# Optimization experiments

Hardware: AMD Instinct MI355X
Metric: run time of the kernel (lower is better)

The kernel has to match this reference:

```python
import jax, jax.numpy as jnp
import numpy as np
from jax import lax

N_NODES, N_EDGES, N_GRAPHS = 102400, 409600, 2048
HID, BN_EPS = 128, 1e-5


def setup_inputs():
    kit = iter(jax.random.split(jax.random.key(0), 64))

    def nrm(shape, s=0.02):
        return jax.random.normal(next(kit), shape, jnp.float32) * s

    inp = {}
    inp["x_ligand"] = jax.random.normal(next(kit), (N_NODES, 78), jnp.float32)
    inp["protein_seq"] = jax.random.normal(next(kit), (N_GRAPHS, 1, 1000), jnp.float32)
    inp["a2h"] = jax.random.normal(next(kit), (N_GRAPHS, 10, 100, 3), jnp.float32)
    inp["edge_index"] = jax.random.randint(next(kit), (2, N_EDGES), 0, N_NODES)
    inp["batch_ligand"] = jnp.sort(jax.random.randint(next(kit), (N_NODES,), 0, N_GRAPHS))
    dins = [78, HID, HID]
    for i in range(3):
        inp[f"gin{i}_W1"] = nrm((dins[i], HID)); inp[f"gin{i}_b1"] = jnp.zeros((HID,), jnp.float32)
        inp[f"gin{i}_W2"] = nrm((HID, HID)); inp[f"gin{i}_b2"] = jnp.zeros((HID,), jnp.float32)
        inp[f"bn{i}_g"] = jnp.ones((HID,), jnp.float32); inp[f"bn{i}_b"] = jnp.zeros((HID,), jnp.float32)
    inp["lig_W"] = nrm((HID, HID)); inp["lig_b"] = jnp.zeros((HID,), jnp.float32)
    inp["conv_k"] = nrm((32, 1, 8)); inp["conv_b"] = jnp.zeros((32,), jnp.float32)
    inp["prot_W"] = nrm((32, HID)); inp["prot_b"] = jnp.zeros((HID,), jnp.float32)
    inp["a2h1_W"] = nrm((3000, HID)); inp["a2h1_b"] = jnp.zeros((HID,), jnp.float32)
    inp["a2h2_W"] = nrm((HID, HID)); inp["a2h2_b"] = jnp.zeros((HID,), jnp.float32)
    inp["c1_W"] = nrm((3 * HID, 2 * HID)); inp["c1_b"] = jnp.zeros((2 * HID,), jnp.float32)
    inp["c2_W"] = nrm((2 * HID, HID)); inp["c2_b"] = jnp.zeros((HID,), jnp.float32)
    inp["out_W"] = nrm((HID, 1)); inp["out_b"] = jnp.zeros((1,), jnp.float32)
    return inp


def _gin_layer(x, src, dst, W1, b1, W2, b2, g, b):
    # scatter-add neighbor aggregation (PyG GINConv, eps=0)
    agg = jax.ops.segment_sum(x[src], dst, num_segments=N_NODES)
    h = x + agg
    h = jax.nn.relu(h @ W1 + b1) @ W2 + b2  # GIN MLP
    mu = h.mean(0)
    var = h.var(0)
    h = (h - mu) * lax.rsqrt(var + BN_EPS) * g + b  # BatchNorm1d (batch stats)
    return jax.nn.relu(h)


def _forward(x_ligand, protein_seq, a2h, edge_index, batch_ligand, gin_params,
             lig_W, lig_b, conv_k, conv_b, prot_W, prot_b,
             a2h1_W, a2h1_b, a2h2_W, a2h2_b, c1_W, c1_b, c2_W, c2_b, out_W, out_b):
    src, dst = edge_index[0], edge_index[1]
    x = x_ligand
    for (W1, b1, W2, b2, g, b) in gin_params:
        x = _gin_layer(x, src, dst, W1, b1, W2, b2, g, b)
    xg = jax.ops.segment_sum(x, batch_ligand, num_segments=N_GRAPHS)  # global_add_pool
    xg = jax.nn.relu(xg @ lig_W + lig_b)
    # protein CNN branch: Conv1d(1->32, k=8) + ReLU + global max pool
    xp = lax.conv_general_dilated(protein_seq, conv_k, (1,), 'VALID',
                                  dimension_numbers=('NCH', 'OIH', 'NCH')) + conv_b[None, :, None]
    xp = jax.nn.relu(xp).max(axis=-1)
    xp = jax.nn.relu(xp @ prot_W + prot_b)
    # a2h MLP branch on flattened trajectory
    xa = a2h.reshape(a2h.shape[0], -1)
    xa = jax.nn.relu(xa @ a2h1_W + a2h1_b)
    xa = jax.nn.relu(xa @ a2h2_W + a2h2_b)
    xc = jnp.concatenate([xg, xp, xa], axis=1)
    xc = jax.nn.relu(xc @ c1_W + c1_b)
    xc = jax.nn.relu(xc @ c2_W + c2_b)
    return xc @ out_W + out_b


def reference(x_ligand, protein_seq, a2h, edge_index, batch_ligand,
              gin0_W1, gin0_b1, gin0_W2, gin0_b2, bn0_g, bn0_b,
              gin1_W1, gin1_b1, gin1_W2, gin1_b2, bn1_g, bn1_b,
              gin2_W1, gin2_b1, gin2_W2, gin2_b2, bn2_g, bn2_b,
              lig_W, lig_b, conv_k, conv_b, prot_W, prot_b,
              a2h1_W, a2h1_b, a2h2_W, a2h2_b, c1_W, c1_b, c2_W, c2_b, out_W, out_b):
    gin_params = [
        (gin0_W1, gin0_b1, gin0_W2, gin0_b2, bn0_g, bn0_b),
        (gin1_W1, gin1_b1, gin1_W2, gin1_b2, bn1_g, bn1_b),
        (gin2_W1, gin2_b1, gin2_W2, gin2_b2, bn2_g, bn2_b),
    ]
    return _forward(x_ligand, protein_seq, a2h, edge_index, batch_ligand, gin_params,
                    lig_W, lig_b, conv_k, conv_b, prot_W, prot_b,
                    a2h1_W, a2h1_b, a2h2_W, a2h2_b, c1_W, c1_b, c2_W, c2_b, out_W, out_b)
```

## Files before the change

kernel.cpp:

```cpp
#include <hip/hip_runtime.h>
#include <math.h>

constexpr int NNODES  = 102400;
constexpr int NEDGES  = 409600;
constexpr int NGRAPHS = 2048;
constexpr int HIDDEN  = 128;

typedef __attribute__((ext_vector_type(8))) short s16x8;
typedef __attribute__((ext_vector_type(4))) float f32x4;

__device__ __forceinline__ float relu_f(float v) { return fmaxf(v, 0.0f); }

__device__ __forceinline__ void split3(float x, short& s0, short& s1, short& s2) {
  unsigned u0 = __float_as_uint(x);
  s0 = (short)(u0 >> 16);
  float r1 = x - __uint_as_float(u0 & 0xFFFF0000u);
  unsigned u1 = __float_as_uint(r1);
  s1 = (short)(u1 >> 16);
  float r2 = r1 - __uint_as_float(u1 & 0xFFFF0000u);
  s2 = (short)(__float_as_uint(r2) >> 16);
}

__global__ void prep_kernel(const int* __restrict__ ei, const int* __restrict__ batch,
                            int* __restrict__ counts, int* __restrict__ gcounts,
                            const float* __restrict__ W10, const float* __restrict__ W20,
                            const float* __restrict__ W11, const float* __restrict__ W21,
                            const float* __restrict__ W12, const float* __restrict__ W22,
                            short* __restrict__ ws) {
  int b = blockIdx.x;
  if (b < NEDGES / 256) {
    atomicAdd(&counts[ei[NEDGES + b * 256 + threadIdx.x]], 1);
    return;
  }
  if (b < NEDGES / 256 + NNODES / 256) {
    atomicAdd(&gcounts[batch[(b - NEDGES / 256) * 256 + threadIdx.x]], 1);
    return;
  }
  int bw = b - (NEDGES / 256 + NNODES / 256);
  int n = threadIdx.x;
  if (n >= 128) return;
  const float* src; long base; int k, realK, KP;
  if (bw < 96) {
    src = W10; base = 0; k = bw; realK = 78; KP = 96;
  } else {
    int q = bw - 96;
    int mat = q >> 7;
    k = q & 127; realK = 128; KP = 128;
    const float* srcs[5] = {W20, W11, W21, W12, W22};
    const long bases[5] = {36864, 86016, 135168, 184320, 233472};
    src = srcs[mat]; base = bases[mat];
  }
  float x = (k < realK) ? src[k * 128 + n] : 0.0f;
  short s0, s1, s2;
  split3(x, s0, s1, s2);
  long e = base + ((long)(k >> 5) * 128 + n) * 32 + (k & 31);
  long ps = (long)KP * 128;
  ws[e] = s0; ws[e + ps] = s1; ws[e + 2 * ps] = s2;
}

__device__ __forceinline__ void scan_block_body(const int* in, int n, int* out_excl,
                                                int* bsums, int lb) {
  __shared__ int s[256];
  int t = threadIdx.x;
  int i = lb * 256 + t;
  int v = (i < n) ? in[i] : 0;
  s[t] = v;
  __syncthreads();
  for (int off = 1; off < 256; off <<= 1) {
    int x = (t >= off) ? s[t - off] : 0;
    __syncthreads();
    s[t] += x;
    __syncthreads();
  }
  if (i < n) out_excl[i] = s[t] - v;
  if (t == 255) bsums[lb] = s[255];
}

__global__ void scan_block2_kernel(const int* __restrict__ counts, int* __restrict__ row_ptr,
                                   int* __restrict__ bsumsA, const int* __restrict__ gcounts,
                                   int* __restrict__ gptr, int* __restrict__ bsumsB) {
  int b = blockIdx.x;
  if (b < NNODES / 256) scan_block_body(counts, NNODES, row_ptr, bsumsA, b);
  else scan_block_body(gcounts, NGRAPHS, gptr, bsumsB, b - NNODES / 256);
}

__global__ void scan_top2_kernel(int* __restrict__ bsumsA, int* __restrict__ bsumsB) {
  __shared__ int s[1024];
  int* bs = (blockIdx.x == 0) ? bsumsA : bsumsB;
  int nb  = (blockIdx.x == 0) ? (NNODES / 256) : (NGRAPHS / 256);
  int t = threadIdx.x;
  int v = (t < nb) ? bs[t] : 0;
  s[t] = v;
  __syncthreads();
  for (int off = 1; off < 1024; off <<= 1) {
    int x = (t >= off) ? s[t - off] : 0;
    __syncthreads();
    s[t] += x;
    __syncthreads();
  }
  if (t < nb) bs[t] = s[t] - v;
  if (t == 1023) bs[nb] = s[1023];
}

__global__ void scan_add2_kernel(int* __restrict__ row_ptr, const int* __restrict__ bsumsA,
                                 int* __restrict__ nxt, int* __restrict__ gptr,
                                 const int* __restrict__ bsumsB) {
  int b = blockIdx.x, t = threadIdx.x;
  if (b < NNODES / 256) {
    int i = b * 256 + t;
    int v = row_ptr[i] + bsumsA[b];
    row_ptr[i] = v;
    nxt[i] = v;
    if (i == 0) row_ptr[NNODES] = bsumsA[NNODES / 256];
  } else {
    int lb = b - NNODES / 256;
    int i = lb * 256 + t;
    gptr[i] += bsumsB[lb];
    if (i == 0) gptr[NGRAPHS] = bsumsB[NGRAPHS / 256];
  }
}

__global__ void scatter_kernel(const int* __restrict__ ei, int* __restrict__ nxt,
                               int* __restrict__ csr_src) {
  int e = blockIdx.x * blockDim.x + threadIdx.x;
  if (e < NEDGES) {
    int s = ei[e];
    int d = ei[NEDGES + e];
    int pos = atomicAdd(&nxt[d], 1);
    csr_src[pos] = s;
  }
}

constexpr int STRK = 132;
template<int DIN, int KP1, bool XF>
__device__ __forceinline__ void gin_block(
    int bid, const float* __restrict__ X,
    const int* __restrict__ row_ptr, const int* __restrict__ csr_src,
    const short* __restrict__ w1s, const float* __restrict__ b1,
    const short* __restrict__ w2s, const float* __restrict__ b2,
    const float* __restrict__ psum, const float* __restrict__ psq,
    const float* __restrict__ bg, const float* __restrict__ bb2,
    float* __restrict__ O, float* __restrict__ bn_sum, float* __restrict__ bn_sq,
    float* buf) {
  const int t = threadIdx.x;
  const int wv = t >> 6, lane = t & 63;
  const int base = bid * 32;

  const int fp = 2 * lane;
  if (fp < KP1) {
    if (fp < DIN) {
      float sc0 = 1.f, sh0 = 0.f, sc1 = 1.f, sh1 = 0.f;
      if (XF) {
        float mu0 = psum[fp] * (1.0f / NNODES);
        float va0 = fmaxf(psq[fp] * (1.0f / NNODES) - mu0 * mu0, 0.0f);
        sc0 = bg[fp] / sqrtf(va0 + 1e-5f);
        sh0 = bb2[fp] - mu0 * sc0;
        float mu1 = psum[fp + 1] * (1.0f / NNODES);
        float va1 = fmaxf(psq[fp + 1] * (1.0f / NNODES) - mu1 * mu1, 0.0f);
        sc1 = bg[fp + 1] / sqrtf(va1 + 1e-5f);
        sh1 = bb2[fp + 1] - mu1 * sc1;
      }
      for (int g = 0; g < 2; ++g) {
        const int rbase = wv * 8 + g * 4;
        float a0[4], a1[4];
        int ecur[4], eend[4], idx[4];
#pragma unroll
        for (int r = 0; r < 4; ++r) {
          const int node = base + rbase + r;
          ecur[r] = row_ptr[node];
          eend[r] = row_ptr[node + 1];
          const float2 s = *(const float2*)&X[(long)node * DIN + fp];
          a0[r] = XF ? relu_f(fmaf(s.x, sc0, sh0)) : s.x;
          a1[r] = XF ? relu_f(fmaf(s.y, sc1, sh1)) : s.y;
          idx[r] = (ecur[r] < eend[r]) ? csr_src[ecur[r]] : -1;
        }
        bool any = (idx[0] >= 0) || (idx[1] >= 0) || (idx[2] >= 0) || (idx[3] >= 0);
        while (any) {
          float2 uu[4];
#pragma unroll
          for (int r = 0; r < 4; ++r)
            if (idx[r] >= 0) uu[r] = *(const float2*)&X[(long)idx[r] * DIN + fp];
          any = false;
#pragma unroll
          for (int r = 0; r < 4; ++r) {
            if (idx[r] >= 0) {
              a0[r] += XF ? relu_f(fmaf(uu[r].x, sc0, sh0)) : uu[r].x;
              a1[r] += XF ? relu_f(fmaf(uu[r].y, sc1, sh1)) : uu[r].y;
              ++ecur[r];
              idx[r] = (ecur[r] < eend[r]) ? csr_src[ecur[r]] : -1;
            }
            any = any || (idx[r] >= 0);
          }
        }
#pragma unroll
        for (int r = 0; r < 4; ++r)
          *(float2*)&buf[(rbase + r) * STRK + fp] = make_float2(a0[r], a1[r]);
      }
    } else {
      for (int r = 0; r < 8; ++r)
        *(float2*)&buf[(wv * 8 + r) * STRK + fp] = make_float2(0.f, 0.f);
    }
  }
  __syncthreads();

  const int rb = wv & 1, nbase = (wv >> 1) * 64;
  const int l15 = lane & 15, quad = lane >> 4;
  const int aoff = (rb * 16 + l15) * STRK;
  constexpr int PS1 = KP1 * 128;
  constexpr int PS2 = 128 * 128;

  f32x4 acc1[4] = {};
  for (int ks = 0; ks < KP1 / 32; ++ks) {
    const int k0 = ks * 32;
    const float4 xa = *(const float4*)&buf[aoff + k0 + quad * 8];
    const float4 xb = *(const float4*)&buf[aoff + k0 + quad * 8 + 4];
    s16x8 A0, A1, A2;
    {
      const float xv[8] = {xa.x, xa.y, xa.z, xa.w, xb.x, xb.y, xb.z, xb.w};
#pragma unroll
      for (int j = 0; j < 8; ++j) {
        short s0, s1, s2;
        split3(xv[j], s0, s1, s2);
        A0[j] = s0; A1[j] = s1; A2[j] = s2;
      }
    }
    s16x8 B0[4], B1[4], B2[4];
#pragma unroll
    for (int ct = 0; ct < 4; ++ct) {
      const int n = nbase + ct * 16 + l15;
      const short* wp = w1s + ((long)(ks * 128 + n) << 5) + (quad << 3);
      B0[ct] = *(const s16x8*)(wp);
      B1[ct] = *(const s16x8*)(wp + PS1);
      B2[ct] = *(const s16x8*)(wp + 2 * PS1);
    }
#pragma unroll
    for (int ct = 0; ct < 4; ++ct) acc1[ct] = __builtin_amdgcn_mfma_f32_16x16x32_bf16(A0, B2[ct], acc1[ct], 0, 0, 0);
#pragma unroll
    for (int ct = 0; ct < 4; ++ct) acc1[ct] = __builtin_amdgcn_mfma_f32_16x16x32_bf16(A1, B1[ct], acc1[ct], 0, 0, 0);
#pragma unroll
    for (int ct = 0; ct < 4; ++ct) acc1[ct] = __builtin_amdgcn_mfma_f32_16x16x32_bf16(A2, B0[ct], acc1[ct], 0, 0, 0);
#pragma unroll
    for (int ct = 0; ct < 4; ++ct) acc1[ct] = __builtin_amdgcn_mfma_f32_16x16x32_bf16(A0, B1[ct], acc1[ct], 0, 0, 0);
#pragma unroll
    for (int ct = 0; ct < 4; ++ct) acc1[ct] = __builtin_amdgcn_mfma_f32_16x16x32_bf16(A1, B0[ct], acc1[ct], 0, 0, 0);
#pragma unroll
    for (int ct = 0; ct < 4; ++ct) acc1[ct] = __builtin_amdgcn_mfma_f32_16x16x32_bf16(A0, B0[ct], acc1[ct], 0, 0, 0);
  }
  __syncthreads();

#pragma unroll
  for (int ct = 0; ct < 4; ++ct) {
    const int n = nbase + ct * 16 + l15;
    const float bb = b1[n];
#pragma unroll
    for (int reg = 0; reg < 4; ++reg) {
      const int m = rb * 16 + quad * 4 + reg;
      buf[m * STRK + n] = relu_f(acc1[ct][reg] + bb);
    }
  }
  __syncthreads();

  f32x4 acc2[4] = {};
  for (int ks = 0; ks < 4; ++ks) {
    const int k0 = ks * 32;
    const float4 xa = *(const float4*)&buf[aoff + k0 + quad * 8];
    const float4 xb = *(const float4*)&buf[aoff + k0 + quad * 8 + 4];
    s16x8 A0, A1, A2;
    {
      const float xv[8] = {xa.x, xa.y, xa.z, xa.w, xb.x, xb.y, xb.z, xb.w};
#pragma unroll
      for (int j = 0; j < 8; ++j) {
        short s0, s1, s2;
        split3(xv[j], s0, s1, s2);
        A0[j] = s0; A1[j] = s1; A2[j] = s2;
      }
    }
    s16x8 B0[4], B1[4], B2[4];
#pragma unroll
    for (int ct = 0; ct < 4; ++ct) {
      const int n = nbase + ct * 16 + l15;
      const short* wp = w2s + ((long)(ks * 128 + n) << 5) + (quad << 3);
      B0[ct] = *(const s16x8*)(wp);
      B1[ct] = *(const s16x8*)(wp + PS2);
      B2[ct] = *(const s16x8*)(wp + 2 * PS2);
    }
#pragma unroll
    for (int ct = 0; ct < 4; ++ct) acc2[ct] = __builtin_amdgcn_mfma_f32_16x16x32_bf16(A0, B2[ct], acc2[ct], 0, 0, 0);
#pragma unroll
    for (int ct = 0; ct < 4; ++ct) acc2[ct] = __builtin_amdgcn_mfma_f32_16x16x32_bf16(A1, B1[ct], acc2[ct], 0, 0, 0);
#pragma unroll
    for (int ct = 0; ct < 4; ++ct) acc2[ct] = __builtin_amdgcn_mfma_f32_16x16x32_bf16(A2, B0[ct], acc2[ct], 0, 0, 0);
#pragma unroll
    for (int ct = 0; ct < 4; ++ct) acc2[ct] = __builtin_amdgcn_mfma_f32_16x16x32_bf16(A0, B1[ct], acc2[ct], 0, 0, 0);
#pragma unroll
    for (int ct = 0; ct < 4; ++ct) acc2[ct] = __builtin_amdgcn_mfma_f32_16x16x32_bf16(A1, B0[ct], acc2[ct], 0, 0, 0);
#pragma unroll
    for (int ct = 0; ct < 4; ++ct) acc2[ct] = __builtin_amdgcn_mfma_f32_16x16x32_bf16(A0, B0[ct], acc2[ct], 0, 0, 0);
  }

  float cs[4], cq[4];
#pragma unroll
  for (int ct = 0; ct < 4; ++ct) {
    const int n = nbase + ct * 16 + l15;
    const float bb = b2[n];
    float s = 0.f, q = 0.f;
#pragma unroll
    for (int reg = 0; reg < 4; ++reg) {
      const int m = rb * 16 + quad * 4 + reg;
      const float o = acc2[ct][reg] + bb;
      O[(long)(base + m) * HIDDEN + n] = o;
      s += o;
      q = fmaf(o, o, q);
    }
    cs[ct] = s; cq[ct] = q;
  }
  __syncthreads();
  const int g = rb * 4 + quad;
#pragma unroll
  for (int ct = 0; ct < 4; ++ct) {
    const int n = nbase + ct * 16 + l15;
    buf[n * 8 + g] = cs[ct];
    buf[1024 + n * 8 + g] = cq[ct];
  }
  __syncthreads();
  if (t < HIDDEN) {
    float s = 0.f, q = 0.f;
    for (int gg = 0; gg < 8; ++gg) { s += buf[t * 8 + gg]; q += buf[1024 + t * 8 + gg]; }
    atomicAdd(&bn_sum[t], s);
    atomicAdd(&bn_sq[t], q);
  }
}

constexpr int A2H_K = 3000, A2H_SPLIT = 200, A2H_NSPLIT = 15;
__device__ __forceinline__ void a2h_block(int rb, int sp, const float* __restrict__ A,
    const float* __restrict__ W, const float* __restrict__ bias, float* __restrict__ XA,
    float* xT) {
  constexpr int STR = 18;
  const int t = threadIdx.x;
  const int row0 = rb * 16;
  const int k0 = sp * A2H_SPLIT;
  for (int i = t; i < 16 * 50; i += 256) {
    const int r = i / 50, kq = i - r * 50;
    const float4 v = *(const float4*)&A[(long)(row0 + r) * A2H_K + k0 + kq * 4];
    xT[(kq * 4 + 0) * STR + r] = v.x;
    xT[(kq * 4 + 1) * STR + r] = v.y;
    xT[(kq * 4 + 2) * STR + r] = v.z;
    xT[(kq * 4 + 3) * STR + r] = v.w;
  }
  __syncthreads();
  const int rg = t >> 5, cg = t & 31;
  const int r0 = rg * 2, j0 = cg * 4;
  float acc[2][4];
  for (int r = 0; r < 2; ++r)
    for (int c = 0; c < 4; ++c) acc[r][c] = 0.f;
  const float* Wp = W + (long)k0 * HIDDEN + j0;
  for (int k = 0; k < A2H_SPLIT; ++k) {
    const float4 w = *(const float4*)&Wp[(long)k * HIDDEN];
    const float2 x = *(const float2*)&xT[k * STR + r0];
    const float wa[4] = {w.x, w.y, w.z, w.w};
    for (int c = 0; c < 4; ++c) {
      acc[0][c] = fmaf(x.x, wa[c], acc[0][c]);
      acc[1][c] = fmaf(x.y, wa[c], acc[1][c]);
    }
  }
  if (sp == 0)
    for (int c = 0; c < 4; ++c) { acc[0][c] += bias[j0 + c]; acc[1][c] += bias[j0 + c]; }
  for (int r = 0; r < 2; ++r)
    for (int c = 0; c < 4; ++c)
      atomicAdd(&XA[(long)(row0 + r0 + r) * HIDDEN + j0 + c], acc[r][c]);
}

__device__ __forceinline__ void conv_block(int g, const float* __restrict__ PS,
    const float* __restrict__ CK, const float* __restrict__ CB, float* __restrict__ XP,
    float* seq) {
  const int t = threadIdx.x;
  for (int i = t; i < 1000; i += 256) seq[i] = PS[g * 1000 + i];
  __syncthreads();
  const int pl = t & 31, cgp = t >> 5;
  float kr[4][8];
  for (int cc = 0; cc < 4; ++cc)
    for (int k = 0; k < 8; ++k) kr[cc][k] = CK[(cgp * 4 + cc) * 8 + k];
  float m[4] = {-1e30f, -1e30f, -1e30f, -1e30f};
  for (int i = 0; i < 32; ++i) {
    int p = pl + 32 * i;
    if (p < 993) {
      float sv[8];
      for (int k = 0; k < 8; ++k) sv[k] = seq[p + k];
      for (int cc = 0; cc < 4; ++cc) {
        float s = 0.f;
        for (int k = 0; k < 8; ++k) s = fmaf(sv[k], kr[cc][k], s);
        m[cc] = fmaxf(m[cc], s);
      }
    }
  }
  for (int off = 16; off >= 1; off >>= 1)
    for (int cc = 0; cc < 4; ++cc) m[cc] = fmaxf(m[cc], __shfl_xor(m[cc], off));
  if (pl == 0)
    for (int cc = 0; cc < 4; ++cc)
      XP[g * 32 + cgp * 4 + cc] = relu_f(m[cc] + CB[cgp * 4 + cc]);
}

__global__ __launch_bounds__(256, 4) void fat0_kernel(
    const float* __restrict__ x_lig, const int* __restrict__ row_ptr,
    const int* __restrict__ csr_src,
    const short* __restrict__ ws, const float* __restrict__ b1,
    const float* __restrict__ b2,
    float* __restrict__ O0, float* __restrict__ bn_sum, float* __restrict__ bn_sq,
    const float* __restrict__ a2h, const float* __restrict__ a1W,
    const float* __restrict__ a1b, float* __restrict__ XA,
    const float* __restrict__ pseq, const float* __restrict__ convk,
    const float* __restrict__ convb, float* __restrict__ XP32) {
  __shared__ __align__(16) float buf[32 * STRK];
  const int b = blockIdx.x;
  if (b < NNODES / 32) {
    gin_block<78, 96, false>(b, x_lig, row_ptr, csr_src, ws, b1, ws + 36864, b2,
                             nullptr, nullptr, nullptr, nullptr, O0, bn_sum, bn_sq, buf);
  } else if (b < NNODES / 32 + (NGRAPHS / 16) * A2H_NSPLIT) {
    const int q = b - NNODES / 32;
    a2h_block(q & 127, q >> 7, a2h, a1W, a1b, XA, buf);
  } else {
    conv_block(b - (NNODES / 32 + (NGRAPHS / 16) * A2H_NSPLIT), pseq, convk, convb, XP32, buf);
  }
}

__global__ __launch_bounds__(256, 4) void gin_kernel(
    const float* __restrict__ X, const int* __restrict__ row_ptr,
    const int* __restrict__ csr_src,
    const short* __restrict__ w1s, const float* __restrict__ b1,
    const short* __restrict__ w2s, const float* __restrict__ b2,
    const float* __restrict__ psum, const float* __restrict__ psq,
    const float* __restrict__ bg, const float* __restrict__ bb2,
    float* __restrict__ O, float* __restrict__ bn_sum, float* __restrict__ bn_sq) {
  __shared__ __align__(16) float buf[32 * STRK];
  gin_block<128, 128, true>(blockIdx.x, X, row_ptr, csr_src, w1s, b1, w2s, b2,
                            psum, psq, bg, bb2, O, bn_sum, bn_sq, buf);
}

__global__ __launch_bounds__(256) void pool_kernel(const float* __restrict__ O,
    const int* __restrict__ gp, const float* __restrict__ psum, const float* __restrict__ psq,
    const float* __restrict__ bg, const float* __restrict__ bb2, float* __restrict__ P) {
  int t = threadIdx.x;
  int g = blockIdx.x * 4 + (t >> 6);
  int lane = t & 63;
  int f0 = lane, f1 = lane + 64;
  float mu0 = psum[f0] * (1.0f / NNODES);
  float va0 = fmaxf(psq[f0] * (1.0f / NNODES) - mu0 * mu0, 0.0f);
  float sc0 = bg[f0] / sqrtf(va0 + 1e-5f);
  float sh0 = bb2[f0] - mu0 * sc0;
  float mu1 = psum[f1] * (1.0f / NNODES);
  float va1 = fmaxf(psq[f1] * (1.0f / NNODES) - mu1 * mu1, 0.0f);
  float sc1 = bg[f1] / sqrtf(va1 + 1e-5f);
  float sh1 = bb2[f1] - mu1 * sc1;
  int n0 = gp[g], n1 = gp[g + 1];
  float a0 = 0.f, a1 = 0.f;
  for (int n = n0; n < n1; ++n) {
    a0 += relu_f(fmaf(O[(long)n * HIDDEN + f0], sc0, sh0));
    a1 += relu_f(fmaf(O[(long)n * HIDDEN + f1], sc1, sh1));
  }
  P[g * HIDDEN + f0] = a0;
  P[g * HIDDEN + f1] = a1;
}

__device__ __forceinline__ void gemm16_body(const float* __restrict__ A, int lda, int K,
    const float* __restrict__ W, int ldw, const float* __restrict__ bias,
    float* __restrict__ C, int ldc, int coff, int yc, bool reluA, float* AT) {
  constexpr int RT = 16, CH = 64, STR = RT + 4;
  const int t = threadIdx.x;
  const int rg = t >> 6, cg = t & 63;
  const int r0 = rg * 4;
  const int row0 = blockIdx.x * RT;
  const int col = yc * 64 + cg;
  float a0 = 0.f, a1 = 0.f, a2 = 0.f, a3 = 0.f;
  for (int k0 = 0; k0 < K; k0 += CH) {
    const int kc = min(CH, K - k0);
    __syncthreads();
    for (int i = t; i < RT * CH; i += 256) {
      int kk = i & (CH - 1), r = i >> 6;
      if (kk < kc) {
        float v = A[(long)(row0 + r) * lda + k0 + kk];
        AT[kk * STR + r] = reluA ? relu_f(v) : v;
      }
    }
    __syncthreads();
    for (int kk = 0; kk < kc; ++kk) {
      const float4 x = *(const float4*)&AT[kk * STR + r0];
      const float w = W[(long)(k0 + kk) * ldw + col];
      a0 = fmaf(x.x, w, a0);
      a1 = fmaf(x.y, w, a1);
      a2 = fmaf(x.z, w, a2);
      a3 = fmaf(x.w, w, a3);
    }
  }
  const float bv = bias[col];
  C[(long)(row0 + r0 + 0) * ldc + coff + col] = relu_f(a0 + bv);
  C[(long)(row0 + r0 + 1) * ldc + coff + col] = relu_f(a1 + bv);
  C[(long)(row0 + r0 + 2) * ldc + coff + col] = relu_f(a2 + bv);
  C[(long)(row0 + r0 + 3) * ldc + coff + col] = relu_f(a3 + bv);
}

__global__ __launch_bounds__(256) void branches_kernel(
    const float* __restrict__ P, const float* __restrict__ XP32, const float* __restrict__ XA,
    const float* __restrict__ ligW, const float* __restrict__ ligb,
    const float* __restrict__ protW, const float* __restrict__ protb,
    const float* __restrict__ a2W, const float* __restrict__ a2b, float* __restrict__ XC) {
  __shared__ __align__(16) float AT[64 * 20];
  const int cfg = blockIdx.y >> 1, yc = blockIdx.y & 1;
  if (cfg == 0)      gemm16_body(P,    128, 128, ligW,  128, ligb,  XC, 384, 0,   yc, false, AT);
  else if (cfg == 1) gemm16_body(XP32, 32,  32,  protW, 128, protb, XC, 384, 128, yc, false, AT);
  else               gemm16_body(XA,   128, 128, a2W,   128, a2b,   XC, 384, 256, yc, true,  AT);
}

__global__ __launch_bounds__(256) void gemm2_kernel(const float* __restrict__ A, int lda, int K,
    const float* __restrict__ W, int ldw, const float* __restrict__ bias,
    float* __restrict__ C, int ldc) {
  __shared__ __align__(16) float AT[64 * 20];
  gemm16_body(A, lda, K, W, ldw, bias, C, ldc, 0, blockIdx.y, false, AT);
}

__global__ __launch_bounds__(256) void final_dot_kernel(const float* __restrict__ X,
    const float* __restrict__ Wo, const float* __restrict__ bo, float* __restrict__ out) {
  int t = threadIdx.x;
  int g = blockIdx.x * 4 + (t >> 6);
  int lane = t & 63;
  float2 x = *(const float2*)&X[g * HIDDEN + lane * 2];
  float2 w = *(const float2*)&Wo[lane * 2];
  float p = x.x * w.x + x.y * w.y;
  for (int off = 32; off >= 1; off >>= 1) p += __shfl_down(p, off);
  if (lane == 0) out[g] = p + bo[0];
}

extern "C" void kernel_launch(void* const* d_in, const int* in_sizes, int n_in,
                              void* d_out, int out_size, void* d_ws, size_t ws_size,
                              hipStream_t stream) {
  const float* x_lig = (const float*)d_in[0];
  const float* pseq  = (const float*)d_in[1];
  const float* a2h   = (const float*)d_in[2];
  const int*   ei    = (const int*)d_in[3];
  const int*   batch = (const int*)d_in[4];
  const float* ginW1[3] = {(const float*)d_in[5],  (const float*)d_in[11], (const float*)d_in[17]};
  const float* ginb1[3] = {(const float*)d_in[6],  (const float*)d_in[12], (const float*)d_in[18]};
  const float* ginW2[3] = {(const float*)d_in[7],  (const float*)d_in[13], (const float*)d_in[19]};
  const float* ginb2[3] = {(const float*)d_in[8],  (const float*)d_in[14], (const float*)d_in[20]};
  const float* bng[3]   = {(const float*)d_in[9],  (const float*)d_in[15], (const float*)d_in[21]};
  const float* bnb[3]   = {(const float*)d_in[10], (const float*)d_in[16], (const float*)d_in[22]};
  const float* ligW  = (const float*)d_in[23]; const float* ligb  = (const float*)d_in[24];
  const float* convk = (const float*)d_in[25]; const float* convb = (const float*)d_in[26];
  const float* protW = (const float*)d_in[27]; const float* protb = (const float*)d_in[28];
  const float* a1W   = (const float*)d_in[29]; const float* a1b   = (const float*)d_in[30];
  const float* a2W   = (const float*)d_in[31]; const float* a2b   = (const float*)d_in[32];
  const float* c1W   = (const float*)d_in[33]; const float* c1b   = (const float*)d_in[34];
  const float* c2W   = (const float*)d_in[35]; const float* c2b   = (const float*)d_in[36];
  const float* oW    = (const float*)d_in[37]; const float* ob    = (const float*)d_in[38];

  char* base = (char*)d_ws;
  size_t off = 0;
  auto alloc = [&](size_t bytes) -> char* {
    char* p = base + off;
    off = (off + bytes + 511) & ~size_t(511);
    return p;
  };
  int*   counts  = (int*)alloc(NNODES * 4);
  int*   gcounts = (int*)alloc(NGRAPHS * 4);
  float* bn_sum  = (float*)alloc(3 * 128 * 4);
  float* bn_sq   = (float*)alloc(3 * 128 * 4);
  float* XA      = (float*)alloc(NGRAPHS * 128 * 4);
  const size_t zero_bytes = off;
  short* wsplit   = (short*)alloc(282624 * 2);
  int*   row_ptr  = (int*)alloc((NNODES + 1) * 4);
  int*   nxt      = (int*)alloc(NNODES * 4);
  int*   gptr     = (int*)alloc((NGRAPHS + 1) * 4);
  int*   bsumsA   = (int*)alloc(401 * 4);
  int*   bsumsB   = (int*)alloc(9 * 4);
  int*   csr_src  = (int*)alloc(NEDGES * 4);
  float* P        = (float*)alloc(NGRAPHS * 128 * 4);
  float* XP32     = (float*)alloc(NGRAPHS * 32 * 4);
  float* XC       = (float*)alloc(NGRAPHS * 384 * 4);
  float* XC2      = (float*)alloc(NGRAPHS * 256 * 4);
  float* XC3      = (float*)alloc(NGRAPHS * 128 * 4);
  float* O0       = (float*)alloc((size_t)NNODES * 128 * 4);
  float* O1       = (float*)alloc((size_t)NNODES * 128 * 4);
  (void)ws_size; (void)in_sizes; (void)n_in; (void)out_size;

  hipMemsetAsync(d_ws, 0, zero_bytes, stream);

  prep_kernel<<<NEDGES / 256 + NNODES / 256 + 736, 256, 0, stream>>>(
      ei, batch, counts, gcounts, ginW1[0], ginW2[0], ginW1[1], ginW2[1],
      ginW1[2], ginW2[2], wsplit);
  scan_block2_kernel<<<NNODES / 256 + NGRAPHS / 256, 256, 0, stream>>>(
      counts, row_ptr, bsumsA, gcounts, gptr, bsumsB);
  scan_top2_kernel<<<2, 1024, 0, stream>>>(bsumsA, bsumsB);
  scan_add2_kernel<<<NNODES / 256 + NGRAPHS / 256, 256, 0, stream>>>(
      row_ptr, bsumsA, nxt, gptr, bsumsB);
  scatter_kernel<<<(NEDGES + 255) / 256, 256, 0, stream>>>(ei, nxt, csr_src);

  fat0_kernel<<<NNODES / 32 + (NGRAPHS / 16) * A2H_NSPLIT + NGRAPHS, 256, 0, stream>>>(
      x_lig, row_ptr, csr_src, wsplit, ginb1[0], ginb2[0],
      O0, bn_sum, bn_sq, a2h, a1W, a1b, XA, pseq, convk, convb, XP32);

  gin_kernel<<<NNODES / 32, 256, 0, stream>>>(O0, row_ptr, csr_src,
      wsplit + 86016, ginb1[1], wsplit + 135168, ginb2[1],
      bn_sum, bn_sq, bng[0], bnb[0], O1, bn_sum + 128, bn_sq + 128);
  gin_kernel<<<NNODES / 32, 256, 0, stream>>>(O1, row_ptr, csr_src,
      wsplit + 184320, ginb1[2], wsplit + 233472, ginb2[2],
      bn_sum + 128, bn_sq + 128, bng[1], bnb[1], O0, bn_sum + 256, bn_sq + 256);

  pool_kernel<<<NGRAPHS / 4, 256, 0, stream>>>(O0, gptr, bn_sum + 256, bn_sq + 256,
                                               bng[2], bnb[2], P);
  branches_kernel<<<dim3(NGRAPHS / 16, 6), 256, 0, stream>>>(
      P, XP32, XA, ligW, ligb, protW, protb, a2W, a2b, XC);
  gemm2_kernel<<<dim3(NGRAPHS / 16, 4), 256, 0, stream>>>(XC, 384, 384, c1W, 256, c1b, XC2, 256);
  gemm2_kernel<<<dim3(NGRAPHS / 16, 2), 256, 0, stream>>>(XC2, 256, 256, c2W, 128, c2b, XC3, 128);
  final_dot_kernel<<<NGRAPHS / 4, 256, 0, stream>>>(XC3, oW, ob, (float*)d_out);
}
```

Before: 848.3 us.

## Fuse pooling and MLP head into one kernel; widen GIN gather to float4

The five tail kernels (pool, three branch linears, two dense layers, final dot) become a single head kernel that does 4 graphs per block and keeps all intermediates in shared memory. This removes launches and global round-trips for P/XC/XC2/XC3. Layers 1-2 of the GIN gather now use float4 loads, with two nodes per wave, instead of float2 loads. The trade-off is that the head kernel rereads every weight matrix for each group of 4 graphs, with only 512 blocks doing scalar FMA loops.

```diff
diff --git a/kernel.cpp b/kernel.cpp
--- a/kernel.cpp
+++ b/kernel.cpp
@@ -132,7 +132,7 @@
 }
 
 constexpr int STRK = 132;
-template<int DIN, int KP1, bool XF>
+template<int DIN, int KP1, bool XF, bool G4>
 __device__ __forceinline__ void gin_block(
     int bid, const float* __restrict__ X,
     const int* __restrict__ row_ptr, const int* __restrict__ csr_src,
@@ -146,59 +146,106 @@
   const int wv = t >> 6, lane = t & 63;
   const int base = bid * 32;
 
-  const int fp = 2 * lane;
-  if (fp < KP1) {
-    if (fp < DIN) {
-      float sc0 = 1.f, sh0 = 0.f, sc1 = 1.f, sh1 = 0.f;
+  if (G4) {
+    const int q = lane & 31, half = lane >> 5;
+    const int f = 4 * q;
+    float sc[4] = {1.f, 1.f, 1.f, 1.f}, sh[4] = {0.f, 0.f, 0.f, 0.f};
+    if (XF) {
+#pragma unroll
+      for (int c = 0; c < 4; ++c) {
+        float mu = psum[f + c] * (1.0f / NNODES);
+        float va = fmaxf(psq[f + c] * (1.0f / NNODES) - mu * mu, 0.0f);
+        sc[c] = bg[f + c] / sqrtf(va + 1e-5f);
+        sh[c] = bb2[f + c] - mu * sc[c];
+      }
+    }
+    float4 acc[4];
+    int ecur[4], eend[4], idx[4];
+#pragma unroll
+    for (int p = 0; p < 4; ++p) {
+      const int node = base + wv * 8 + 2 * p + half;
+      ecur[p] = row_ptr[node];
+      eend[p] = row_ptr[node + 1];
+      float4 s = *(const float4*)&X[(long)node * 128 + f];
       if (XF) {
-        float mu0 = psum[fp] * (1.0f / NNODES);
-        float va0 = fmaxf(psq[fp] * (1.0f / NNODES) - mu0 * mu0, 0.0f);
-        sc0 = bg[fp] / sqrtf(va0 + 1e-5f);
-        sh0 = bb2[fp] - mu0 * sc0;
-        float mu1 = psum[fp + 1] * (1.0f / NNODES);
-        float va1 = fmaxf(psq[fp + 1] * (1.0f / NNODES) - mu1 * mu1, 0.0f);
-        sc1 = bg[fp + 1] / sqrtf(va1 + 1e-5f);
-        sh1 = bb2[fp + 1] - mu1 * sc1;
+        acc[p].x = relu_f(fmaf(s.x, sc[0], sh[0]));
+        acc[p].y = relu_f(fmaf(s.y, sc[1], sh[1]));
+        acc[p].z = relu_f(fmaf(s.z, sc[2], sh[2]));
+        acc[p].w = relu_f(fmaf(s.w, sc[3], sh[3]));
+      } else acc[p] = s;
+      idx[p] = (ecur[p] < eend[p]) ? csr_src[ecur[p]] : -1;
+    }
+    bool any = (idx[0] >= 0) || (idx[1] >= 0) || (idx[2] >= 0) || (idx[3] >= 0);
+    while (any) {
+      float4 uu[4];
+#pragma unroll
+      for (int p = 0; p < 4; ++p)
+        if (idx[p] >= 0) uu[p] = *(const float4*)&X[(long)idx[p] * 128 + f];
+      any = false;
+#pragma unroll
+      for (int p = 0; p < 4; ++p) {
+        if (idx[p] >= 0) {
+          if (XF) {
+            acc[p].x += relu_f(fmaf(uu[p].x, sc[0], sh[0]));
+            acc[p].y += relu_f(fmaf(uu[p].y, sc[1], sh[1]));
+            acc[p].z += relu_f(fmaf(uu[p].z, sc[2], sh[2]));
+            acc[p].w += relu_f(fmaf(uu[p].w, sc[3], sh[3]));
+          } else {
+            acc[p].x += uu[p].x; acc[p].y += uu[p].y;
+            acc[p].z += uu[p].z; acc[p].w += uu[p].w;
+          }
+          ++ecur[p];
+          idx[p] = (ecur[p] < eend[p]) ? csr_src[ecur[p]] : -1;
+        }
+        any = any || (idx[p] >= 0);
       }
-      for (int g = 0; g < 2; ++g) {
-        const int rbase = wv * 8 + g * 4;
-        float a0[4], a1[4];
-        int ecur[4], eend[4], idx[4];
-#pragma unroll
-        for (int r = 0; r < 4; ++r) {
-          const int node = base + rbase + r;
-          ecur[r] = row_ptr[node];
-          eend[r] = row_ptr[node + 1];
-          const float2 s = *(const float2*)&X[(long)node * DIN + fp];
-          a0[r] = XF ? relu_f(fmaf(s.x, sc0, sh0)) : s.x;
-          a1[r] = XF ? relu_f(fmaf(s.y, sc1, sh1)) : s.y;
-          idx[r] = (ecur[r] < eend[r]) ? csr_src[ecur[r]] : -1;
+    }
+#pragma unroll
+    for (int p = 0; p < 4; ++p)
+      *(float4*)&buf[(wv * 8 + 2 * p + half) * STRK + f] = acc[p];
+  } else {
+    const int fp = 2 * lane;
+    if (fp < KP1) {
+      if (fp < DIN) {
+        for (int g = 0; g < 2; ++g) {
+          const int rbase = wv * 8 + g * 4;
+          float a0[4], a1[4];
+          int ecur[4], eend[4], idx[4];
+#pragma unroll
+          for (int r = 0; r < 4; ++r) {
+            const int node = base + rbase + r;
+            ecur[r] = row_ptr[node];
+            eend[r] = row_ptr[node + 1];
+            const float2 s = *(const float2*)&X[(long)node * DIN + fp];
+            a0[r] = s.x; a1[r] = s.y;
+            idx[r] = (ecur[r] < eend[r]) ? csr_src[ecur[r]] : -1;
+          }
+          bool any = (idx[0] >= 0) || (idx[1] >= 0) || (idx[2] >= 0) || (idx[3] >= 0);
+          while (any) {
+            float2 uu[4];
+#pragma unroll
+            for (int r = 0; r < 4; ++r)
+              if (idx[r] >= 0) uu[r] = *(const float2*)&X[(long)idx[r] * DIN + fp];
+            any = false;
+#pragma unroll
+            for (int r = 0; r < 4; ++r) {
+              if (idx[r] >= 0) {
+                a0[r] += uu[r].x;
+                a1[r] += uu[r].y;
+                ++ecur[r];
+                idx[r] = (ecur[r] < eend[r]) ? csr_src[ecur[r]] : -1;
+              }
+              any = any || (idx[r] >= 0);
+            }
+          }
+#pragma unroll
+          for (int r = 0; r < 4; ++r)
+            *(float2*)&buf[(rbase + r) * STRK + fp] = make_float2(a0[r], a1[r]);
         }
-        bool any = (idx[0] >= 0) || (idx[1] >= 0) || (idx[2] >= 0) || (idx[3] >= 0);
-        while (any) {
-          float2 uu[4];
-#pragma unroll
-          for (int r = 0; r < 4; ++r)
-            if (idx[r] >= 0) uu[r] = *(const float2*)&X[(long)idx[r] * DIN + fp];
-          any = false;
-#pragma unroll
-          for (int r = 0; r < 4; ++r) {
-            if (idx[r] >= 0) {
-              a0[r] += XF ? relu_f(fmaf(uu[r].x, sc0, sh0)) : uu[r].x;
-              a1[r] += XF ? relu_f(fmaf(uu[r].y, sc1, sh1)) : uu[r].y;
-              ++ecur[r];
-              idx[r] = (ecur[r] < eend[r]) ? csr_src[ecur[r]] : -1;
-            }
-            any = any || (idx[r] >= 0);
-          }
-        }
-#pragma unroll
-        for (int r = 0; r < 4; ++r)
-          *(float2*)&buf[(rbase + r) * STRK + fp] = make_float2(a0[r], a1[r]);
+      } else {
+        for (int r = 0; r < 8; ++r)
+          *(float2*)&buf[(wv * 8 + r) * STRK + fp] = make_float2(0.f, 0.f);
       }
-    } else {
-      for (int r = 0; r < 8; ++r)
-        *(float2*)&buf[(wv * 8 + r) * STRK + fp] = make_float2(0.f, 0.f);
     }
   }
   __syncthreads();
@@ -413,8 +460,8 @@
   __shared__ __align__(16) float buf[32 * STRK];
   const int b = blockIdx.x;
   if (b < NNODES / 32) {
-    gin_block<78, 96, false>(b, x_lig, row_ptr, csr_src, ws, b1, ws + 36864, b2,
-                             nullptr, nullptr, nullptr, nullptr, O0, bn_sum, bn_sq, buf);
+    gin_block<78, 96, false, false>(b, x_lig, row_ptr, csr_src, ws, b1, ws + 36864, b2,
+                                    nullptr, nullptr, nullptr, nullptr, O0, bn_sum, bn_sq, buf);
   } else if (b < NNODES / 32 + (NGRAPHS / 16) * A2H_NSPLIT) {
     const int q = b - NNODES / 32;
     a2h_block(q & 127, q >> 7, a2h, a1W, a1b, XA, buf);
@@ -432,101 +479,111 @@
     const float* __restrict__ bg, const float* __restrict__ bb2,
     float* __restrict__ O, float* __restrict__ bn_sum, float* __restrict__ bn_sq) {
   __shared__ __align__(16) float buf[32 * STRK];
-  gin_block<128, 128, true>(blockIdx.x, X, row_ptr, csr_src, w1s, b1, w2s, b2,
-                            psum, psq, bg, bb2, O, bn_sum, bn_sq, buf);
-}
-
-__global__ __launch_bounds__(256) void pool_kernel(const float* __restrict__ O,
-    const int* __restrict__ gp, const float* __restrict__ psum, const float* __restrict__ psq,
-    const float* __restrict__ bg, const float* __restrict__ bb2, float* __restrict__ P) {
-  int t = threadIdx.x;
-  int g = blockIdx.x * 4 + (t >> 6);
-  int lane = t & 63;
-  int f0 = lane, f1 = lane + 64;
-  float mu0 = psum[f0] * (1.0f / NNODES);
-  float va0 = fmaxf(psq[f0] * (1.0f / NNODES) - mu0 * mu0, 0.0f);
-  float sc0 = bg[f0] / sqrtf(va0 + 1e-5f);
-  float sh0 = bb2[f0] - mu0 * sc0;
-  float mu1 = psum[f1] * (1.0f / NNODES);
-  float va1 = fmaxf(psq[f1] * (1.0f / NNODES) - mu1 * mu1, 0.0f);
-  float sc1 = bg[f1] / sqrtf(va1 + 1e-5f);
-  float sh1 = bb2[f1] - mu1 * sc1;
-  int n0 = gp[g], n1 = gp[g + 1];
-  float a0 = 0.f, a1 = 0.f;
-  for (int n = n0; n < n1; ++n) {
-    a0 += relu_f(fmaf(O[(long)n * HIDDEN + f0], sc0, sh0));
-    a1 += relu_f(fmaf(O[(long)n * HIDDEN + f1], sc1, sh1));
-  }
-  P[g * HIDDEN + f0] = a0;
-  P[g * HIDDEN + f1] = a1;
-}
-
-__device__ __forceinline__ void gemm16_body(const float* __restrict__ A, int lda, int K,
-    const float* __restrict__ W, int ldw, const float* __restrict__ bias,
-    float* __restrict__ C, int ldc, int coff, int yc, bool reluA, float* AT) {
-  constexpr int RT = 16, CH = 64, STR = RT + 4;
-  const int t = threadIdx.x;
-  const int rg = t >> 6, cg = t & 63;
-  const int r0 = rg * 4;
-  const int row0 = blockIdx.x * RT;
-  const int col = yc * 64 + cg;
-  float a0 = 0.f, a1 = 0.f, a2 = 0.f, a3 = 0.f;
-  for (int k0 = 0; k0 < K; k0 += CH) {
-    const int kc = min(CH, K - k0);
-    __syncthreads();
-    for (int i = t; i < RT * CH; i += 256) {
-      int kk = i & (CH - 1), r = i >> 6;
-      if (kk < kc) {
-        float v = A[(long)(row0 + r) * lda + k0 + kk];
-        AT[kk * STR + r] = reluA ? relu_f(v) : v;
-      }
-    }
-    __syncthreads();
-    for (int kk = 0; kk < kc; ++kk) {
-      const float4 x = *(const float4*)&AT[kk * STR + r0];
-      const float w = W[(long)(k0 + kk) * ldw + col];
-      a0 = fmaf(x.x, w, a0);
-      a1 = fmaf(x.y, w, a1);
-      a2 = fmaf(x.z, w, a2);
-      a3 = fmaf(x.w, w, a3);
-    }
-  }
-  const float bv = bias[col];
-  C[(long)(row0 + r0 + 0) * ldc + coff + col] = relu_f(a0 + bv);
-  C[(long)(row0 + r0 + 1) * ldc + coff + col] = relu_f(a1 + bv);
-  C[(long)(row0 + r0 + 2) * ldc + coff + col] = relu_f(a2 + bv);
-  C[(long)(row0 + r0 + 3) * ldc + coff + col] = relu_f(a3 + bv);
-}
-
-__global__ __launch_bounds__(256) void branches_kernel(
-    const float* __restrict__ P, const float* __restrict__ XP32, const float* __restrict__ XA,
+  gin_block<128, 128, true, true>(blockIdx.x, X, row_ptr, csr_src, w1s, b1, w2s, b2,
+                                  psum, psq, bg, bb2, O, bn_sum, bn_sq, buf);
+}
+
+__global__ __launch_bounds__(256) void head_kernel(
+    const float* __restrict__ O, const int* __restrict__ gp,
+    const float* __restrict__ psum, const float* __restrict__ psq,
+    const float* __restrict__ bg, const float* __restrict__ bb2,
+    const float* __restrict__ XP32, const float* __restrict__ XA,
     const float* __restrict__ ligW, const float* __restrict__ ligb,
     const float* __restrict__ protW, const float* __restrict__ protb,
-    const float* __restrict__ a2W, const float* __restrict__ a2b, float* __restrict__ XC) {
-  __shared__ __align__(16) float AT[64 * 20];
-  const int cfg = blockIdx.y >> 1, yc = blockIdx.y & 1;
-  if (cfg == 0)      gemm16_body(P,    128, 128, ligW,  128, ligb,  XC, 384, 0,   yc, false, AT);
-  else if (cfg == 1) gemm16_body(XP32, 32,  32,  protW, 128, protb, XC, 384, 128, yc, false, AT);
-  else               gemm16_body(XA,   128, 128, a2W,   128, a2b,   XC, 384, 256, yc, true,  AT);
-}
-
-__global__ __launch_bounds__(256) void gemm2_kernel(const float* __restrict__ A, int lda, int K,
-    const float* __restrict__ W, int ldw, const float* __restrict__ bias,
-    float* __restrict__ C, int ldc) {
-  __shared__ __align__(16) float AT[64 * 20];
-  gemm16_body(A, lda, K, W, ldw, bias, C, ldc, 0, blockIdx.y, false, AT);
-}
-
-__global__ __launch_bounds__(256) void final_dot_kernel(const float* __restrict__ X,
-    const float* __restrict__ Wo, const float* __restrict__ bo, float* __restrict__ out) {
-  int t = threadIdx.x;
-  int g = blockIdx.x * 4 + (t >> 6);
-  int lane = t & 63;
-  float2 x = *(const float2*)&X[g * HIDDEN + lane * 2];
-  float2 w = *(const float2*)&Wo[lane * 2];
-  float p = x.x * w.x + x.y * w.y;
-  for (int off = 32; off >= 1; off >>= 1) p += __shfl_down(p, off);
-  if (lane == 0) out[g] = p + bo[0];
+    const float* __restrict__ a2W, const float* __restrict__ a2b,
+    const float* __restrict__ c1W, const float* __restrict__ c1b,
+    const float* __restrict__ c2W, const float* __restrict__ c2b,
+    const float* __restrict__ oW, const float* __restrict__ ob,
+    float* __restrict__ out) {
+  __shared__ float Ps[4][128];
+  __shared__ float XAs[4][128];
+  __shared__ float XPs[4][32];
+  __shared__ float XCs[4][384];
+  __shared__ float XC2s[4][256];
+  __shared__ float XC3s[4][128];
+  const int t = threadIdx.x;
+  const int g0 = blockIdx.x * 4;
+
+  {
+    const int sub = t >> 6, lane = t & 63;
+    const int g = g0 + sub;
+    const int f0 = lane, f1 = lane + 64;
+    float mu0 = psum[f0] * (1.0f / NNODES);
+    float va0 = fmaxf(psq[f0] * (1.0f / NNODES) - mu0 * mu0, 0.0f);
+    float sc0 = bg[f0] / sqrtf(va0 + 1e-5f);
+    float sh0 = bb2[f0] - mu0 * sc0;
+    float mu1 = psum[f1] * (1.0f / NNODES);
+    float va1 = fmaxf(psq[f1] * (1.0f / NNODES) - mu1 * mu1, 0.0f);
+    float sc1 = bg[f1] / sqrtf(va1 + 1e-5f);
+    float sh1 = bb2[f1] - mu1 * sc1;
+    const int n0 = gp[g], n1 = gp[g + 1];
+    float a0 = 0.f, a1 = 0.f;
+    for (int n = n0; n < n1; ++n) {
+      a0 += relu_f(fmaf(O[(long)n * HIDDEN + f0], sc0, sh0));
+      a1 += relu_f(fmaf(O[(long)n * HIDDEN + f1], sc1, sh1));
+    }
+    Ps[sub][f0] = a0;
+    Ps[sub][f1] = a1;
+    for (int i = t; i < 512; i += 256) XAs[i >> 7][i & 127] = relu_f(XA[g0 * 128 + i]);
+    for (int i = t; i < 128; i += 256) XPs[i >> 5][i & 31] = XP32[g0 * 32 + i];
+  }
+  __syncthreads();
+
+  {
+    const int j = t & 127, pr = t >> 7;
+    const int s0 = pr * 2, s1 = pr * 2 + 1;
+    float L0 = ligb[j], L1 = L0;
+    float A0 = a2b[j], A1 = A0;
+    for (int k = 0; k < 128; ++k) {
+      const float wl = ligW[k * 128 + j];
+      const float wa = a2W[k * 128 + j];
+      L0 = fmaf(Ps[s0][k], wl, L0); L1 = fmaf(Ps[s1][k], wl, L1);
+      A0 = fmaf(XAs[s0][k], wa, A0); A1 = fmaf(XAs[s1][k], wa, A1);
+    }
+    float P0 = protb[j], P1 = P0;
+    for (int k = 0; k < 32; ++k) {
+      const float wp = protW[k * 128 + j];
+      P0 = fmaf(XPs[s0][k], wp, P0); P1 = fmaf(XPs[s1][k], wp, P1);
+    }
+    XCs[s0][j] = relu_f(L0);        XCs[s1][j] = relu_f(L1);
+    XCs[s0][128 + j] = relu_f(P0);  XCs[s1][128 + j] = relu_f(P1);
+    XCs[s0][256 + j] = relu_f(A0);  XCs[s1][256 + j] = relu_f(A1);
+  }
+  __syncthreads();
+
+  {
+    const int j = t;
+    float a[4];
+    const float bv = c1b[j];
+    for (int s = 0; s < 4; ++s) a[s] = bv;
+    for (int k = 0; k < 384; ++k) {
+      const float w = c1W[k * 256 + j];
+      for (int s = 0; s < 4; ++s) a[s] = fmaf(XCs[s][k], w, a[s]);
+    }
+    for (int s = 0; s < 4; ++s) XC2s[s][j] = relu_f(a[s]);
+  }
+  __syncthreads();
+
+  {
+    const int j = t & 127, pr = t >> 7;
+    const int s0 = pr * 2, s1 = pr * 2 + 1;
+    float a0 = c2b[j], a1 = a0;
+    for (int k = 0; k < 256; ++k) {
+      const float w = c2W[k * 128 + j];
+      a0 = fmaf(XC2s[s0][k], w, a0);
+      a1 = fmaf(XC2s[s1][k], w, a1);
+    }
+    XC3s[s0][j] = relu_f(a0);
+    XC3s[s1][j] = relu_f(a1);
+  }
+  __syncthreads();
+
+  {
+    const int w = t >> 6, lane = t & 63;
+    float p = XC3s[w][lane] * oW[lane] + XC3s[w][lane + 64] * oW[lane + 64];
+    for (int off = 32; off >= 1; off >>= 1) p += __shfl_down(p, off);
+    if (lane == 0) out[g0 + w] = p + ob[0];
+  }
 }
 
 extern "C" void kernel_launch(void* const* d_in, const int* in_sizes, int n_in,
@@ -572,11 +629,7 @@
   int*   bsumsA   = (int*)alloc(401 * 4);
   int*   bsumsB   = (int*)alloc(9 * 4);
   int*   csr_src  = (int*)alloc(NEDGES * 4);
-  float* P        = (float*)alloc(NGRAPHS * 128 * 4);
   float* XP32     = (float*)alloc(NGRAPHS * 32 * 4);
-  float* XC       = (float*)alloc(NGRAPHS * 384 * 4);
-  float* XC2      = (float*)alloc(NGRAPHS * 256 * 4);
-  float* XC3      = (float*)alloc(NGRAPHS * 128 * 4);
   float* O0       = (float*)alloc((size_t)NNODES * 128 * 4);
   float* O1       = (float*)alloc((size_t)NNODES * 128 * 4);
   (void)ws_size; (void)in_sizes; (void)n_in; (void)out_size;
@@ -604,11 +657,7 @@
       wsplit + 184320, ginb1[2], wsplit + 233472, ginb2[2],
       bn_sum + 128, bn_sq + 128, bng[1], bnb[1], O0, bn_sum + 256, bn_sq + 256);
 
-  pool_kernel<<<NGRAPHS / 4, 256, 0, stream>>>(O0, gptr, bn_sum + 256, bn_sq + 256,
-                                               bng[2], bnb[2], P);
-  branches_kernel<<<dim3(NGRAPHS / 16, 6), 256, 0, stream>>>(
-      P, XP32, XA, ligW, ligb, protW, protb, a2W, a2b, XC);
-  gemm2_kernel<<<dim3(NGRAPHS / 16, 4), 256, 0, stream>>>(XC, 384, 384, c1W, 256, c1b, XC2, 256);
-  gemm2_kernel<<<dim3(NGRAPHS / 16, 2), 256, 0, stream>>>(XC2, 256, 256, c2W, 128, c2b, XC3, 128);
-  final_dot_kernel<<<NGRAPHS / 4, 256, 0, stream>>>(XC3, oW, ob, (float*)d_out);
-}
+  head_kernel<<<NGRAPHS / 4, 256, 0, stream>>>(O0, gptr,
+      bn_sum + 256, bn_sq + 256, bng[2], bnb[2], XP32, XA,
+      ligW, ligb, protW, protb, a2W, a2b, c1W, c1b, c2W, c2b, oW, ob, (float*)d_out);
+}
```

Result: faster. 764.7 us (-9.9%).
